# Kernel optimization log

Measured on AMD Instinct MI355X. Metric: run time of the kernel, lower is better.

The kernel has to match this reference:

```python
import jax, jax.numpy as jnp
import numpy as np

B, N, D, K = 64, 4096, 256, 32


def setup_inputs() -> dict:
    key = jax.random.key(0)
    kx, kc, ks = jax.random.split(key, 3)
    x = jax.random.normal(kx, (B, N, D), dtype=jnp.float32)
    # codebook: 'orthogonal' init approximated by normalized gaussian rows
    C = jax.random.normal(kc, (K, D), dtype=jnp.float32) / np.sqrt(D)
    # keras 'uniform' initializer: U(-0.05, 0.05)
    S = jax.random.uniform(ks, (K,), dtype=jnp.float32, minval=-0.05, maxval=0.05)
    return {"x": x, "C": C, "S": S}


def reference(x, C, S):
    """Deep-TEN encoding.
    r_ik = x_i - C_k ;  w = softmax_k(-S_k * ||r_ik||^2) ;  E_k = sum_i w_ik * r_ik.
    ||r||^2 expanded as ||x||^2 - 2 x.C + ||C||^2 to avoid the [B,N,K,D] residual;
    aggregation likewise split: E = einsum(w, x) - (sum_i w) * C.
    """
    x2 = jnp.sum(x * x, axis=-1, keepdims=True)          # [B,N,1]
    c2 = jnp.sum(C * C, axis=-1)                         # [K]
    xc = jnp.einsum('bnd,kd->bnk', x, C)                 # [B,N,K]
    dist = x2 - 2.0 * xc + c2                            # [B,N,K] = ||x_i - C_k||^2
    w = jax.nn.softmax(-S * dist, axis=-1)               # [B,N,K]
    # E_k = sum_i w_ik * (x_i - C_k)
    E = jnp.einsum('bnk,bnd->bkd', w, x) - jnp.sum(w, axis=1)[..., None] * C
    return E                                             # [B,K,D]
```

## Files before the change

### kernel.cpp

```cpp
#include <hip/hip_runtime.h>
#include <stdint.h>


#define NN 4096
#define DD 256
#define KK 32

typedef __attribute__((ext_vector_type(8))) short short8;
typedef __attribute__((ext_vector_type(4))) float float4v;

__device__ __forceinline__ unsigned short f2bf(float f) {
    unsigned u = __float_as_uint(f);
    unsigned r = (u + 0x7fffu + ((u >> 16) & 1u)) >> 16;
    return (unsigned short)r;
}
__device__ __forceinline__ unsigned pk2(float a, float b) {
    return (unsigned)f2bf(a) | ((unsigned)f2bf(b) << 16);
}
__device__ __forceinline__ short8 pack8(float4 a, float4 b) {
    short8 r;
    r[0] = (short)f2bf(a.x); r[1] = (short)f2bf(a.y);
    r[2] = (short)f2bf(a.z); r[3] = (short)f2bf(a.w);
    r[4] = (short)f2bf(b.x); r[5] = (short)f2bf(b.y);
    r[6] = (short)f2bf(b.z); r[7] = (short)f2bf(b.w);
    return r;
}

__launch_bounds__(256)
__global__ void dten_kernel(const float* __restrict__ X,
                            const float* __restrict__ Cg,
                            const float* __restrict__ Sg,
                            float* __restrict__ out) {
    const int b     = blockIdx.y;
    const int chunk = blockIdx.x;
    const int tid   = threadIdx.x;
    const int lane  = tid & 63;
    const int wv    = tid >> 6;
    const int lk    = lane & 15;
    const int lq    = lane >> 4;
    const int rp = tid & 15;
    const int dc = tid >> 4;
    const int nt = wv >> 1;
    const int kt = wv & 1;

    __shared__ __align__(16) unsigned short xa[32 * 264];
    __shared__ __align__(16) unsigned short xt[256 * 40];
    __shared__ __align__(16) unsigned short wt[32 * 40];
    __shared__ __align__(16) float x2p[4][32];
    __shared__ __align__(16) float mex[2][32];
    __shared__ __align__(16) float sex[2][32];
    __shared__ __align__(16) float wsum_p[2][32];

    const int kA = kt * 16 + lk;
    short8 cfrag[8];
    float c2k;
    {
        const float* crow = Cg + (size_t)kA * DD;
        float c2part = 0.f;
        #pragma unroll
        for (int ch = 0; ch < 8; ++ch) {
            float4 u0 = *(const float4*)(crow + ch * 32 + lq * 8);
            float4 u1 = *(const float4*)(crow + ch * 32 + lq * 8 + 4);
            cfrag[ch] = pack8(u0, u1);
            c2part += u0.x*u0.x + u0.y*u0.y + u0.z*u0.z + u0.w*u0.w
                    + u1.x*u1.x + u1.y*u1.y + u1.z*u1.z + u1.w*u1.w;
        }
        c2part += __shfl_xor(c2part, 16);
        c2part += __shfl_xor(c2part, 32);
        c2k = c2part;
    }
    const float sk = Sg[kA];

    float4v eacc[2][4];
    #pragma unroll
    for (int i = 0; i < 2; ++i)
        #pragma unroll
        for (int j = 0; j < 4; ++j)
            eacc[i][j] = (float4v){0.f, 0.f, 0.f, 0.f};
    float wsum_reg = 0.f;

    const int row_base = chunk * 256;
    const int n0 = nt * 16;
    const int nl = n0 + lk;

    for (int t = 0; t < 8; ++t) {
        const int row0 = row_base + t * 32;
        __syncthreads();

        const size_t xoff = ((size_t)b * NN + row0 + 2 * rp) * DD + dc * 16;
        const float4* xr0 = (const float4*)(X + xoff);
        const float4* xr1 = (const float4*)(X + xoff + DD);
        float4 v0[4], v1[4];
        #pragma unroll
        for (int i = 0; i < 4; ++i) { v0[i] = xr0[i]; v1[i] = xr1[i]; }

        float s0 = 0.f, s1 = 0.f;
        #pragma unroll
        for (int i = 0; i < 4; ++i) {
            s0 += v0[i].x*v0[i].x + v0[i].y*v0[i].y + v0[i].z*v0[i].z + v0[i].w*v0[i].w;
            s1 += v1[i].x*v1[i].x + v1[i].y*v1[i].y + v1[i].z*v1[i].z + v1[i].w*v1[i].w;
        }
        s0 += __shfl_xor(s0, 16); s0 += __shfl_xor(s0, 32);
        s1 += __shfl_xor(s1, 16); s1 += __shfl_xor(s1, 32);
        if (lane < 16) { x2p[wv][2 * rp] = s0; x2p[wv][2 * rp + 1] = s1; }

        {
            const int na = 2 * rp, nb = 2 * rp + 1;
            *(short8*)&xa[na * 264 + dc * 16    ] = pack8(v0[0], v0[1]);
            *(short8*)&xa[na * 264 + dc * 16 + 8] = pack8(v0[2], v0[3]);
            *(short8*)&xa[nb * 264 + dc * 16    ] = pack8(v1[0], v1[1]);
            *(short8*)&xa[nb * 264 + dc * 16 + 8] = pack8(v1[2], v1[3]);
        }
        {
            const float* f0 = (const float*)v0;
            const float* f1 = (const float*)v1;
            #pragma unroll
            for (int m = 0; m < 16; ++m) {
                int d = dc * 16 + m;
                *(unsigned*)&xt[d * 40 + 2 * rp] = pk2(f0[m], f1[m]);
            }
        }
        __syncthreads();

        float4v acc = (float4v){0.f, 0.f, 0.f, 0.f};
        #pragma unroll
        for (int ch = 0; ch < 8; ++ch) {
            short8 af = *(const short8*)&xa[nl * 264 + ch * 32 + lq * 8];
            acc = __builtin_amdgcn_mfma_f32_16x16x32_bf16(af, cfrag[ch], acc, 0, 0, 0);
        }
        float4 xs0 = *(const float4*)&x2p[0][n0 + lq * 4];
        float4 xs1 = *(const float4*)&x2p[1][n0 + lq * 4];
        float4 xs2 = *(const float4*)&x2p[2][n0 + lq * 4];
        float4 xs3 = *(const float4*)&x2p[3][n0 + lq * 4];
        float xsum[4] = { xs0.x + xs1.x + xs2.x + xs3.x,
                          xs0.y + xs1.y + xs2.y + xs3.y,
                          xs0.z + xs1.z + xs2.z + xs3.z,
                          xs0.w + xs1.w + xs2.w + xs3.w };
        float a[4], ml[4];
        #pragma unroll
        for (int r = 0; r < 4; ++r) {
            a[r] = sk * (2.f * acc[r] - xsum[r] - c2k);
            ml[r] = a[r];
        }
        #pragma unroll
        for (int mask = 1; mask <= 8; mask <<= 1)
            #pragma unroll
            for (int r = 0; r < 4; ++r)
                ml[r] = fmaxf(ml[r], __shfl_xor(ml[r], mask));
        float e[4], sl[4];
        #pragma unroll
        for (int r = 0; r < 4; ++r) { e[r] = __expf(a[r] - ml[r]); sl[r] = e[r]; }
        #pragma unroll
        for (int mask = 1; mask <= 8; mask <<= 1)
            #pragma unroll
            for (int r = 0; r < 4; ++r)
                sl[r] += __shfl_xor(sl[r], mask);
        if (lk == 0) {
            *(float4*)&mex[kt][n0 + lq * 4] = make_float4(ml[0], ml[1], ml[2], ml[3]);
            *(float4*)&sex[kt][n0 + lq * 4] = make_float4(sl[0], sl[1], sl[2], sl[3]);
        }
        __syncthreads();
        float4 mo4 = *(const float4*)&mex[1 - kt][n0 + lq * 4];
        float4 so4 = *(const float4*)&sex[1 - kt][n0 + lq * 4];
        float mo[4] = { mo4.x, mo4.y, mo4.z, mo4.w };
        float so[4] = { so4.x, so4.y, so4.z, so4.w };
        float w[4];
        #pragma unroll
        for (int r = 0; r < 4; ++r) {
            float M   = fmaxf(ml[r], mo[r]);
            float sc  = __expf(ml[r] - M);
            float den = sl[r] * sc + so[r] * __expf(mo[r] - M);
            w[r] = e[r] * sc / den;
        }
        float ws = w[0] + w[1] + w[2] + w[3];
        ws += __shfl_xor(ws, 16); ws += __shfl_xor(ws, 32);
        wsum_reg += ws;
        *(uint2*)&wt[kA * 40 + n0 + lq * 4] = make_uint2(pk2(w[0], w[1]), pk2(w[2], w[3]));
        __syncthreads();

        short8 af0 = *(const short8*)&wt[lk * 40 + lq * 8];
        short8 af1 = *(const short8*)&wt[(16 + lk) * 40 + lq * 8];
        #pragma unroll
        for (int dt = 0; dt < 4; ++dt) {
            int d = wv * 64 + dt * 16 + lk;
            short8 bf = *(const short8*)&xt[d * 40 + lq * 8];
            eacc[0][dt] = __builtin_amdgcn_mfma_f32_16x16x32_bf16(af0, bf, eacc[0][dt], 0, 0, 0);
            eacc[1][dt] = __builtin_amdgcn_mfma_f32_16x16x32_bf16(af1, bf, eacc[1][dt], 0, 0, 0);
        }
    }

    if (lq == 0) wsum_p[nt][kA] = wsum_reg;
    __syncthreads();
    #pragma unroll
    for (int kt2 = 0; kt2 < 2; ++kt2) {
        #pragma unroll
        for (int r = 0; r < 4; ++r) {
            int k = kt2 * 16 + lq * 4 + r;
            float wsk = wsum_p[0][k] + wsum_p[1][k];
            #pragma unroll
            for (int dt = 0; dt < 4; ++dt) {
                int d = wv * 64 + dt * 16 + lk;
                float cv = Cg[k * DD + d];
                float val = eacc[kt2][dt][r] - wsk * cv;
                unsafeAtomicAdd(&out[((size_t)b * KK + k) * DD + d], val);
            }
        }
    }
}

extern "C" void kernel_launch(void* const* d_in, const int* in_sizes, int n_in,
                              void* d_out, int out_size, void* d_ws, size_t ws_size,
                              hipStream_t stream) {
    const float* X = (const float*)d_in[0];
    const float* C = (const float*)d_in[1];
    const float* S = (const float*)d_in[2];
    float* out = (float*)d_out;
    hipMemsetAsync(out, 0, (size_t)out_size * sizeof(float), stream);
    dim3 grid(16, 64);
    dten_kernel<<<grid, dim3(256), 0, stream>>>(X, C, S, out);
}
```

Before: 399.9 us.

## Restructure tile to 64 rows with per-wave full-K softmax and swizzled LDS

Tiles grow from 32 to 64 rows per iteration. Each wave now computes the x·C scores for all 32 codewords on its own 16 rows, which drops the cross-wave max/sum exchange and one barrier per tile. The transposed xt copy goes away: x is stored once in an XOR-swizzled layout and the aggregation B operand is gathered element by element from it. Row norms use DPP reductions, launch bounds request 2 blocks per CU, and the gathered scalar LDS reads may add LDS instruction pressure.

```diff
diff --git a/kernel.cpp b/kernel.cpp
--- a/kernel.cpp
+++ b/kernel.cpp
@@ -11,8 +11,7 @@
 
 __device__ __forceinline__ unsigned short f2bf(float f) {
     unsigned u = __float_as_uint(f);
-    unsigned r = (u + 0x7fffu + ((u >> 16) & 1u)) >> 16;
-    return (unsigned short)r;
+    return (unsigned short)((u + 0x7fffu + ((u >> 16) & 1u)) >> 16);
 }
 __device__ __forceinline__ unsigned pk2(float a, float b) {
     return (unsigned)f2bf(a) | ((unsigned)f2bf(b) << 16);
@@ -25,8 +24,13 @@
     r[6] = (short)f2bf(b.z); r[7] = (short)f2bf(b.w);
     return r;
 }
-
-__launch_bounds__(256)
+__device__ __forceinline__ int swx(int n) { return (n & 7) ^ ((n >> 2) & 6); }
+
+#define DPP_ADD(v, ctrl) \
+    ((v) + __int_as_float(__builtin_amdgcn_update_dpp( \
+        0, __float_as_int(v), (ctrl), 0xf, 0xf, true)))
+
+__launch_bounds__(256, 2)
 __global__ void dten_kernel(const float* __restrict__ X,
                             const float* __restrict__ Cg,
                             const float* __restrict__ Sg,
@@ -38,38 +42,55 @@
     const int wv    = tid >> 6;
     const int lk    = lane & 15;
     const int lq    = lane >> 4;
-    const int rp = tid & 15;
-    const int dc = tid >> 4;
-    const int nt = wv >> 1;
-    const int kt = wv & 1;
-
-    __shared__ __align__(16) unsigned short xa[32 * 264];
-    __shared__ __align__(16) unsigned short xt[256 * 40];
-    __shared__ __align__(16) unsigned short wt[32 * 40];
-    __shared__ __align__(16) float x2p[4][32];
-    __shared__ __align__(16) float mex[2][32];
-    __shared__ __align__(16) float sex[2][32];
-    __shared__ __align__(16) float wsum_p[2][32];
-
-    const int kA = kt * 16 + lk;
-    short8 cfrag[8];
-    float c2k;
+
+    __shared__ __align__(16) unsigned short xa[64 * 256];
+    __shared__ __align__(16) unsigned short wt[32 * 64];
+    __shared__ __align__(16) float x2s[64];
+    __shared__ __align__(16) float c2p[8][32];
+    __shared__ __align__(16) float c2s[32];
+    __shared__ __align__(16) float wss[4][32];
+
     {
-        const float* crow = Cg + (size_t)kA * DD;
-        float c2part = 0.f;
+        int k = tid & 31, seg = tid >> 5;
+        const float4* cr = (const float4*)(Cg + k * DD + seg * 32);
+        float p = 0.f;
+        #pragma unroll
+        for (int i = 0; i < 8; ++i) {
+            float4 u = cr[i];
+            p += u.x*u.x + u.y*u.y + u.z*u.z + u.w*u.w;
+        }
+        c2p[seg][k] = p;
+    }
+    __syncthreads();
+    if (tid < 32) {
+        float s = 0.f;
+        #pragma unroll
+        for (int seg = 0; seg < 8; ++seg) s += c2p[seg][tid];
+        c2s[tid] = s;
+    }
+    __syncthreads();
+
+    float sk8[8], c2k8[8];
+    #pragma unroll
+    for (int kt = 0; kt < 2; ++kt)
+        #pragma unroll
+        for (int r = 0; r < 4; ++r) {
+            int k = 16 * kt + 4 * lq + r;
+            sk8[kt * 4 + r]  = Sg[k];
+            c2k8[kt * 4 + r] = c2s[k];
+        }
+
+    short8 cfrag[2][8];
+    #pragma unroll
+    for (int kt = 0; kt < 2; ++kt) {
+        const float* crow = Cg + (size_t)(16 * kt + lk) * DD + lq * 8;
         #pragma unroll
         for (int ch = 0; ch < 8; ++ch) {
-            float4 u0 = *(const float4*)(crow + ch * 32 + lq * 8);
-            float4 u1 = *(const float4*)(crow + ch * 32 + lq * 8 + 4);
-            cfrag[ch] = pack8(u0, u1);
-            c2part += u0.x*u0.x + u0.y*u0.y + u0.z*u0.z + u0.w*u0.w
-                    + u1.x*u1.x + u1.y*u1.y + u1.z*u1.z + u1.w*u1.w;
-        }
-        c2part += __shfl_xor(c2part, 16);
-        c2part += __shfl_xor(c2part, 32);
-        c2k = c2part;
-    }
-    const float sk = Sg[kA];
+            float4 u0 = *(const float4*)(crow + ch * 32);
+            float4 u1 = *(const float4*)(crow + ch * 32 + 4);
+            cfrag[kt][ch] = pack8(u0, u1);
+        }
+    }
 
     float4v eacc[2][4];
     #pragma unroll
@@ -77,131 +98,119 @@
         #pragma unroll
         for (int j = 0; j < 4; ++j)
             eacc[i][j] = (float4v){0.f, 0.f, 0.f, 0.f};
-    float wsum_reg = 0.f;
+    float wsr[8] = {0.f, 0.f, 0.f, 0.f, 0.f, 0.f, 0.f, 0.f};
 
     const int row_base = chunk * 256;
-    const int n0 = nt * 16;
-    const int nl = n0 + lk;
-
-    for (int t = 0; t < 8; ++t) {
-        const int row0 = row_base + t * 32;
+    const int nown = 16 * wv + lk;
+
+    for (int t = 0; t < 4; ++t) {
+        const int row0 = row_base + t * 64;
         __syncthreads();
 
-        const size_t xoff = ((size_t)b * NN + row0 + 2 * rp) * DD + dc * 16;
-        const float4* xr0 = (const float4*)(X + xoff);
-        const float4* xr1 = (const float4*)(X + xoff + DD);
-        float4 v0[4], v1[4];
-        #pragma unroll
-        for (int i = 0; i < 4; ++i) { v0[i] = xr0[i]; v1[i] = xr1[i]; }
-
-        float s0 = 0.f, s1 = 0.f;
-        #pragma unroll
-        for (int i = 0; i < 4; ++i) {
-            s0 += v0[i].x*v0[i].x + v0[i].y*v0[i].y + v0[i].z*v0[i].z + v0[i].w*v0[i].w;
-            s1 += v1[i].x*v1[i].x + v1[i].y*v1[i].y + v1[i].z*v1[i].z + v1[i].w*v1[i].w;
-        }
-        s0 += __shfl_xor(s0, 16); s0 += __shfl_xor(s0, 32);
-        s1 += __shfl_xor(s1, 16); s1 += __shfl_xor(s1, 32);
-        if (lane < 16) { x2p[wv][2 * rp] = s0; x2p[wv][2 * rp + 1] = s1; }
-
+        const float4* xt4 = (const float4*)(X + ((size_t)b * NN + row0) * DD);
+        #pragma unroll
+        for (int it = 0; it < 16; ++it) {
+            int rl = wv * 16 + it;
+            float4 v = xt4[rl * 64 + lane];
+            float p = v.x*v.x + v.y*v.y + v.z*v.z + v.w*v.w;
+            p = DPP_ADD(p, 0x111); p = DPP_ADD(p, 0x112);
+            p = DPP_ADD(p, 0x114); p = DPP_ADD(p, 0x118);
+            p = DPP_ADD(p, 0x142); p = DPP_ADD(p, 0x143);
+            if (lane == 63) x2s[rl] = p;
+            int cs = (lane >> 1) ^ swx(rl);
+            uint2 w2 = make_uint2(pk2(v.x, v.y), pk2(v.z, v.w));
+            *(uint2*)&xa[rl * 256 + cs * 8 + 4 * (lane & 1)] = w2;
+        }
+
+        float4v a0 = (float4v){0.f, 0.f, 0.f, 0.f};
+        float4v a1 = (float4v){0.f, 0.f, 0.f, 0.f};
         {
-            const int na = 2 * rp, nb = 2 * rp + 1;
-            *(short8*)&xa[na * 264 + dc * 16    ] = pack8(v0[0], v0[1]);
-            *(short8*)&xa[na * 264 + dc * 16 + 8] = pack8(v0[2], v0[3]);
-            *(short8*)&xa[nb * 264 + dc * 16    ] = pack8(v1[0], v1[1]);
-            *(short8*)&xa[nb * 264 + dc * 16 + 8] = pack8(v1[2], v1[3]);
-        }
+            const int rowoff = nown * 256;
+            const int s = swx(nown);
+            #pragma unroll
+            for (int ch = 0; ch < 8; ++ch) {
+                int c = (4 * ch + lq) ^ s;
+                short8 bf = *(const short8*)&xa[rowoff + c * 8];
+                a0 = __builtin_amdgcn_mfma_f32_16x16x32_bf16(cfrag[0][ch], bf, a0, 0, 0, 0);
+                a1 = __builtin_amdgcn_mfma_f32_16x16x32_bf16(cfrag[1][ch], bf, a1, 0, 0, 0);
+            }
+        }
+        float x2n = x2s[nown];
+        float aa[8];
+        #pragma unroll
+        for (int r = 0; r < 4; ++r) {
+            aa[r]     = sk8[r]     * (2.f * a0[r] - x2n - c2k8[r]);
+            aa[4 + r] = sk8[4 + r] * (2.f * a1[r] - x2n - c2k8[4 + r]);
+        }
+        float m = aa[0];
+        #pragma unroll
+        for (int i = 1; i < 8; ++i) m = fmaxf(m, aa[i]);
+        m = fmaxf(m, __shfl_xor(m, 16));
+        m = fmaxf(m, __shfl_xor(m, 32));
+        float e[8], den = 0.f;
+        #pragma unroll
+        for (int i = 0; i < 8; ++i) { e[i] = __expf(aa[i] - m); den += e[i]; }
+        den += __shfl_xor(den, 16);
+        den += __shfl_xor(den, 32);
+        float inv = __builtin_amdgcn_rcpf(den);
         {
-            const float* f0 = (const float*)v0;
-            const float* f1 = (const float*)v1;
-            #pragma unroll
-            for (int m = 0; m < 16; ++m) {
-                int d = dc * 16 + m;
-                *(unsigned*)&xt[d * 40 + 2 * rp] = pk2(f0[m], f1[m]);
+            const int nhi = nown >> 3, nlo = nown & 7;
+            #pragma unroll
+            for (int i = 0; i < 8; ++i) {
+                float w = e[i] * inv;
+                wsr[i] += w;
+                int k = 16 * (i >> 2) + 4 * lq + (i & 3);
+                wt[k * 64 + ((nhi ^ (k & 7)) << 3) + nlo] = f2bf(w);
             }
         }
         __syncthreads();
 
-        float4v acc = (float4v){0.f, 0.f, 0.f, 0.f};
-        #pragma unroll
-        for (int ch = 0; ch < 8; ++ch) {
-            short8 af = *(const short8*)&xa[nl * 264 + ch * 32 + lq * 8];
-            acc = __builtin_amdgcn_mfma_f32_16x16x32_bf16(af, cfrag[ch], acc, 0, 0, 0);
-        }
-        float4 xs0 = *(const float4*)&x2p[0][n0 + lq * 4];
-        float4 xs1 = *(const float4*)&x2p[1][n0 + lq * 4];
-        float4 xs2 = *(const float4*)&x2p[2][n0 + lq * 4];
-        float4 xs3 = *(const float4*)&x2p[3][n0 + lq * 4];
-        float xsum[4] = { xs0.x + xs1.x + xs2.x + xs3.x,
-                          xs0.y + xs1.y + xs2.y + xs3.y,
-                          xs0.z + xs1.z + xs2.z + xs3.z,
-                          xs0.w + xs1.w + xs2.w + xs3.w };
-        float a[4], ml[4];
+        #pragma unroll
+        for (int nc = 0; nc < 2; ++nc) {
+            int nf = nc * 4 + lq;
+            short8 af0 = *(const short8*)&wt[lk * 64 + ((nf ^ (lk & 7)) << 3)];
+            short8 af1 = *(const short8*)&wt[(16 + lk) * 64 + ((nf ^ (lk & 7)) << 3)];
+            #pragma unroll
+            for (int dt = 0; dt < 4; ++dt) {
+                int cb = 8 * wv + 2 * dt + (lk >> 3);
+                short8 bf;
+                #pragma unroll
+                for (int j = 0; j < 8; ++j) {
+                    int n2 = nc * 32 + lq * 8 + j;
+                    bf[j] = (short)xa[n2 * 256 + ((cb ^ swx(n2)) << 3) + (lk & 7)];
+                }
+                eacc[0][dt] = __builtin_amdgcn_mfma_f32_16x16x32_bf16(af0, bf, eacc[0][dt], 0, 0, 0);
+                eacc[1][dt] = __builtin_amdgcn_mfma_f32_16x16x32_bf16(af1, bf, eacc[1][dt], 0, 0, 0);
+            }
+        }
+    }
+
+    #pragma unroll
+    for (int i = 0; i < 8; ++i) {
+        wsr[i] += __shfl_xor(wsr[i], 1);
+        wsr[i] += __shfl_xor(wsr[i], 2);
+        wsr[i] += __shfl_xor(wsr[i], 4);
+        wsr[i] += __shfl_xor(wsr[i], 8);
+    }
+    if (lk == 0) {
+        #pragma unroll
+        for (int i = 0; i < 8; ++i) {
+            int k = 16 * (i >> 2) + 4 * lq + (i & 3);
+            wss[wv][k] = wsr[i];
+        }
+    }
+    __syncthreads();
+
+    #pragma unroll
+    for (int kt = 0; kt < 2; ++kt) {
         #pragma unroll
         for (int r = 0; r < 4; ++r) {
-            a[r] = sk * (2.f * acc[r] - xsum[r] - c2k);
-            ml[r] = a[r];
-        }
-        #pragma unroll
-        for (int mask = 1; mask <= 8; mask <<= 1)
-            #pragma unroll
-            for (int r = 0; r < 4; ++r)
-                ml[r] = fmaxf(ml[r], __shfl_xor(ml[r], mask));
-        float e[4], sl[4];
-        #pragma unroll
-        for (int r = 0; r < 4; ++r) { e[r] = __expf(a[r] - ml[r]); sl[r] = e[r]; }
-        #pragma unroll
-        for (int mask = 1; mask <= 8; mask <<= 1)
-            #pragma unroll
-            for (int r = 0; r < 4; ++r)
-                sl[r] += __shfl_xor(sl[r], mask);
-        if (lk == 0) {
-            *(float4*)&mex[kt][n0 + lq * 4] = make_float4(ml[0], ml[1], ml[2], ml[3]);
-            *(float4*)&sex[kt][n0 + lq * 4] = make_float4(sl[0], sl[1], sl[2], sl[3]);
-        }
-        __syncthreads();
-        float4 mo4 = *(const float4*)&mex[1 - kt][n0 + lq * 4];
-        float4 so4 = *(const float4*)&sex[1 - kt][n0 + lq * 4];
-        float mo[4] = { mo4.x, mo4.y, mo4.z, mo4.w };
-        float so[4] = { so4.x, so4.y, so4.z, so4.w };
-        float w[4];
-        #pragma unroll
-        for (int r = 0; r < 4; ++r) {
-            float M   = fmaxf(ml[r], mo[r]);
-            float sc  = __expf(ml[r] - M);
-            float den = sl[r] * sc + so[r] * __expf(mo[r] - M);
-            w[r] = e[r] * sc / den;
-        }
-        float ws = w[0] + w[1] + w[2] + w[3];
-        ws += __shfl_xor(ws, 16); ws += __shfl_xor(ws, 32);
-        wsum_reg += ws;
-        *(uint2*)&wt[kA * 40 + n0 + lq * 4] = make_uint2(pk2(w[0], w[1]), pk2(w[2], w[3]));
-        __syncthreads();
-
-        short8 af0 = *(const short8*)&wt[lk * 40 + lq * 8];
-        short8 af1 = *(const short8*)&wt[(16 + lk) * 40 + lq * 8];
-        #pragma unroll
-        for (int dt = 0; dt < 4; ++dt) {
-            int d = wv * 64 + dt * 16 + lk;
-            short8 bf = *(const short8*)&xt[d * 40 + lq * 8];
-            eacc[0][dt] = __builtin_amdgcn_mfma_f32_16x16x32_bf16(af0, bf, eacc[0][dt], 0, 0, 0);
-            eacc[1][dt] = __builtin_amdgcn_mfma_f32_16x16x32_bf16(af1, bf, eacc[1][dt], 0, 0, 0);
-        }
-    }
-
-    if (lq == 0) wsum_p[nt][kA] = wsum_reg;
-    __syncthreads();
-    #pragma unroll
-    for (int kt2 = 0; kt2 < 2; ++kt2) {
-        #pragma unroll
-        for (int r = 0; r < 4; ++r) {
-            int k = kt2 * 16 + lq * 4 + r;
-            float wsk = wsum_p[0][k] + wsum_p[1][k];
+            int k = 16 * kt + 4 * lq + r;
+            float wsk = wss[0][k] + wss[1][k] + wss[2][k] + wss[3][k];
             #pragma unroll
             for (int dt = 0; dt < 4; ++dt) {
-                int d = wv * 64 + dt * 16 + lk;
-                float cv = Cg[k * DD + d];
-                float val = eacc[kt2][dt][r] - wsk * cv;
+                int d = 64 * wv + 16 * dt + lk;
+                float val = eacc[kt][dt][r] - wsk * Cg[(size_t)k * DD + d];
                 unsafeAtomicAdd(&out[((size_t)b * KK + k) * DD + d], val);
             }
         }
```

Measured after the change: 424.0 us. 1.06x slower.
